# Kernel optimization log

Hardware: AMD Instinct MI355X
Metric: run time of the kernel (lower is better)

Reference implementation:

```python
import jax, jax.numpy as jnp
import numpy as np

STRIDE = 1
PADDING = 1

def setup_inputs() -> dict:
    key = jax.random.key(0)
    k1, k2 = jax.random.split(key)
    X = jax.random.normal(k1, (32, 1024, 1024), dtype=jnp.float32)
    weight = jnp.array([[-1.0, -1.0, -1.0], [-1.0, 8.0, -1.0], [-1.0, -1.0, -1.0]], dtype=jnp.float32)
    return {"X": X, "weight": weight}

def reference(X, weight):
    # single-channel 2D cross-correlation, stride=1, padding=1
    # X: [B, M, N] -> lhs [B, 1, M, N]; weight: [u, v] -> rhs [1, 1, u, v]
    lhs = X[:, None, :, :]
    rhs = weight[None, None, :, :]
    out = jax.lax.conv_general_dilated(
        lhs, rhs,
        window_strides=(STRIDE, STRIDE),
        padding=[(PADDING, PADDING), (PADDING, PADDING)],
        dimension_numbers=("NCHW", "OIHW", "NCHW"),
    )
    return out[:, 0, :, :]  # [B, out_h, out_w]
```

## Files before the change

### kernel.cpp

```cpp
#include <hip/hip_runtime.h>

#define IMG_W 1024
#define IMG_H 1024
#define BATCH 32

__global__ __launch_bounds__(256) void conv3x3_kernel(
    const float* __restrict__ X,
    const float* __restrict__ wt,
    float* __restrict__ out)
{
    const int y  = blockIdx.x;
    const int b  = blockIdx.y;
    const int c0 = threadIdx.x * 4;

    const float* img = X + (size_t)b * IMG_H * IMG_W;
    float* orow = out + ((size_t)b * IMG_H + y) * IMG_W + c0;

    const float w0 = wt[0], w1 = wt[1], w2 = wt[2];
    const float w3 = wt[3], w4 = wt[4], w5 = wt[5];
    const float w6 = wt[6], w7 = wt[7], w8 = wt[8];

    float T[6], M[6], B[6];

    {
        int ry = y - 1;
        if (ry < 0) {
            T[0]=T[1]=T[2]=T[3]=T[4]=T[5]=0.f;
        } else {
            const float* p = img + (size_t)ry * IMG_W + c0;
            float4 v = *(const float4*)p;
            T[1]=v.x; T[2]=v.y; T[3]=v.z; T[4]=v.w;
            T[0] = (c0 > 0)           ? p[-1] : 0.f;
            T[5] = (c0 + 4 < IMG_W)   ? p[4]  : 0.f;
        }
    }
    {
        const float* p = img + (size_t)y * IMG_W + c0;
        float4 v = *(const float4*)p;
        M[1]=v.x; M[2]=v.y; M[3]=v.z; M[4]=v.w;
        M[0] = (c0 > 0)           ? p[-1] : 0.f;
        M[5] = (c0 + 4 < IMG_W)   ? p[4]  : 0.f;
    }
    {
        int ry = y + 1;
        if (ry >= IMG_H) {
            B[0]=B[1]=B[2]=B[3]=B[4]=B[5]=0.f;
        } else {
            const float* p = img + (size_t)ry * IMG_W + c0;
            float4 v = *(const float4*)p;
            B[1]=v.x; B[2]=v.y; B[3]=v.z; B[4]=v.w;
            B[0] = (c0 > 0)           ? p[-1] : 0.f;
            B[5] = (c0 + 4 < IMG_W)   ? p[4]  : 0.f;
        }
    }

    float4 r;
    float* rp = &r.x;
#pragma unroll
    for (int j = 0; j < 4; ++j) {
        rp[j] = w0*T[j] + w1*T[j+1] + w2*T[j+2]
              + w3*M[j] + w4*M[j+1] + w5*M[j+2]
              + w6*B[j] + w7*B[j+1] + w8*B[j+2];
    }

    *(float4*)orow = r;
}

extern "C" void kernel_launch(void* const* d_in, const int* in_sizes, int n_in,
                              void* d_out, int out_size, void* d_ws, size_t ws_size,
                              hipStream_t stream) {
    const float* X  = (const float*)d_in[0];
    const float* wt = (const float*)d_in[1];
    float* out = (float*)d_out;

    dim3 grid(IMG_H, BATCH);
    dim3 block(256);
    conv3x3_kernel<<<grid, block, 0, stream>>>(X, wt, out);
}
```

Baseline: 246.8 us.

## Compute eight output rows per thread to reuse loaded input rows

Each thread now loads ten input rows into registers and produces eight output rows, instead of reloading three rows for every single output row. This cuts redundant global and cache reads and issues more independent loads per thread. Output writes use nontemporal stores so the cache is not polluted. The costs are higher register use and fewer blocks in the grid.

New measurement: 229.6 us. 1.08x faster.

```diff
diff --git a/kernel.cpp b/kernel.cpp
--- a/kernel.cpp
+++ b/kernel.cpp
@@ -3,67 +3,54 @@
 #define IMG_W 1024
 #define IMG_H 1024
 #define BATCH 32
+#define ROWS 8
+
+typedef float vfloat4 __attribute__((ext_vector_type(4)));
 
 __global__ __launch_bounds__(256) void conv3x3_kernel(
     const float* __restrict__ X,
     const float* __restrict__ wt,
     float* __restrict__ out)
 {
-    const int y  = blockIdx.x;
+    const int y0 = blockIdx.x * ROWS;
     const int b  = blockIdx.y;
     const int c0 = threadIdx.x * 4;
 
     const float* img = X + (size_t)b * IMG_H * IMG_W;
-    float* orow = out + ((size_t)b * IMG_H + y) * IMG_W + c0;
 
     const float w0 = wt[0], w1 = wt[1], w2 = wt[2];
     const float w3 = wt[3], w4 = wt[4], w5 = wt[5];
     const float w6 = wt[6], w7 = wt[7], w8 = wt[8];
 
-    float T[6], M[6], B[6];
+    float R[ROWS + 2][6];
 
-    {
-        int ry = y - 1;
-        if (ry < 0) {
-            T[0]=T[1]=T[2]=T[3]=T[4]=T[5]=0.f;
+#pragma unroll
+    for (int i = 0; i < ROWS + 2; ++i) {
+        const int ry = y0 + i - 1;
+        if (ry >= 0 && ry < IMG_H) {
+            const float* p = img + (size_t)ry * IMG_W + c0;
+            const vfloat4 v = *(const vfloat4*)p;
+            R[i][1] = v.x; R[i][2] = v.y; R[i][3] = v.z; R[i][4] = v.w;
+            R[i][0] = (c0 > 0)         ? p[-1] : 0.f;
+            R[i][5] = (c0 + 4 < IMG_W) ? p[4]  : 0.f;
         } else {
-            const float* p = img + (size_t)ry * IMG_W + c0;
-            float4 v = *(const float4*)p;
-            T[1]=v.x; T[2]=v.y; T[3]=v.z; T[4]=v.w;
-            T[0] = (c0 > 0)           ? p[-1] : 0.f;
-            T[5] = (c0 + 4 < IMG_W)   ? p[4]  : 0.f;
-        }
-    }
-    {
-        const float* p = img + (size_t)y * IMG_W + c0;
-        float4 v = *(const float4*)p;
-        M[1]=v.x; M[2]=v.y; M[3]=v.z; M[4]=v.w;
-        M[0] = (c0 > 0)           ? p[-1] : 0.f;
-        M[5] = (c0 + 4 < IMG_W)   ? p[4]  : 0.f;
-    }
-    {
-        int ry = y + 1;
-        if (ry >= IMG_H) {
-            B[0]=B[1]=B[2]=B[3]=B[4]=B[5]=0.f;
-        } else {
-            const float* p = img + (size_t)ry * IMG_W + c0;
-            float4 v = *(const float4*)p;
-            B[1]=v.x; B[2]=v.y; B[3]=v.z; B[4]=v.w;
-            B[0] = (c0 > 0)           ? p[-1] : 0.f;
-            B[5] = (c0 + 4 < IMG_W)   ? p[4]  : 0.f;
+            R[i][0] = R[i][1] = R[i][2] = R[i][3] = R[i][4] = R[i][5] = 0.f;
         }
     }
 
-    float4 r;
-    float* rp = &r.x;
+    float* obase = out + ((size_t)b * IMG_H + y0) * IMG_W + c0;
+
 #pragma unroll
-    for (int j = 0; j < 4; ++j) {
-        rp[j] = w0*T[j] + w1*T[j+1] + w2*T[j+2]
-              + w3*M[j] + w4*M[j+1] + w5*M[j+2]
-              + w6*B[j] + w7*B[j+1] + w8*B[j+2];
+    for (int i = 0; i < ROWS; ++i) {
+        vfloat4 r;
+#pragma unroll
+        for (int j = 0; j < 4; ++j) {
+            r[j] = w0 * R[i][j]     + w1 * R[i][j + 1]     + w2 * R[i][j + 2]
+                 + w3 * R[i + 1][j] + w4 * R[i + 1][j + 1] + w5 * R[i + 1][j + 2]
+                 + w6 * R[i + 2][j] + w7 * R[i + 2][j + 1] + w8 * R[i + 2][j + 2];
+        }
+        __builtin_nontemporal_store(r, (vfloat4*)(obase + (size_t)i * IMG_W));
     }
-
-    *(float4*)orow = r;
 }
 
 extern "C" void kernel_launch(void* const* d_in, const int* in_sizes, int n_in,
@@ -73,7 +60,7 @@
     const float* wt = (const float*)d_in[1];
     float* out = (float*)d_out;
 
-    dim3 grid(IMG_H, BATCH);
+    dim3 grid(IMG_H / ROWS, BATCH);
     dim3 block(256);
     conv3x3_kernel<<<grid, block, 0, stream>>>(X, wt, out);
 }
```
